# Optimization experiments

Hardware: AMD Instinct MI355X
Metric: run time of the kernel (lower is better)

## Reference

```python
import jax, jax.numpy as jnp
import numpy as np

NUM_CLASSES = 100
CLUSTERS_PER_CLASS = 64
LATENT_DIM = 128
BATCH = 32768


def setup_inputs() -> dict:
    key = jax.random.key(0)
    kx, kc, kl = jax.random.split(key, 3)
    x = jax.random.normal(kx, (BATCH, LATENT_DIM), dtype=jnp.float32)
    # nn.Parameter(torch.randn(C, Kc, D) * 0.1)
    centers = jax.random.normal(kc, (NUM_CLASSES, CLUSTERS_PER_CLASS, LATENT_DIM), dtype=jnp.float32) * 0.1
    labels = jax.random.randint(kl, (BATCH,), 0, NUM_CLASSES, dtype=jnp.int64)
    return {"x": x, "centers": centers, "labels": labels}


def reference(x, centers, labels):
    # [C, Kc, D] -> [K, D]
    all_centers = centers.reshape(-1, LATENT_DIM).astype(x.dtype)
    x2 = jnp.sum(x * x, axis=-1, keepdims=True)            # [B,1]
    c2 = jnp.sum(all_centers * all_centers, axis=-1)       # [K]
    sq = x2 + c2[None, :] - 2.0 * jnp.einsum('bd,kd->bk', x, all_centers)
    distances = jnp.sqrt(jnp.maximum(sq, 0.0))             # [B,K]
    closest_indices = jnp.argmin(distances, axis=1)        # [B]
    class_predictions = closest_indices // CLUSTERS_PER_CLASS
    cluster_assignments = closest_indices % CLUSTERS_PER_CLASS
    quantized_hard = all_centers[closest_indices]          # [B,D]
    min_distances = jnp.take_along_axis(distances, closest_indices[:, None], axis=1)[:, 0]
    # straight-through estimator (training path in the torch module)
    quantized = x + jax.lax.stop_gradient(quantized_hard - x)
    return quantized, cluster_assignments, min_distances, class_predictions
```

## Files before the change

### kernel.cpp

```cpp
#include <hip/hip_runtime.h>
#include <math.h>

#define BATCH  32768
#define D      128
#define K      6400
#define KC     64
#define ROWS_PER_BLOCK 128
#define CHUNK_C 128
#define NCHUNKS 50

typedef _Float16 half8 __attribute__((ext_vector_type(8)));
typedef float    floatx4 __attribute__((ext_vector_type(4)));

typedef __attribute__((address_space(3))) unsigned       lds_uint;
typedef __attribute__((address_space(1))) const unsigned glb_uint;

__device__ __forceinline__ void async_lds16(const void* g, void* l) {
    __builtin_amdgcn_global_load_lds((glb_uint*)g, (lds_uint*)l, 16, 0, 0);
}

__global__ __launch_bounds__(256) void pack_kernel(const float* __restrict__ centers,
                                                   _Float16* __restrict__ wh,
                                                   float* __restrict__ c2n) {
    int tid = blockIdx.x * 256 + threadIdx.x;
    int ch = tid >> 11;
    int u  = (tid >> 7) & 15;
    int cw = tid & 127;
    int center = ch * CHUNK_C + cw;
    const float* src = centers + (size_t)center * D + u * 8;
    float4 a = *(const float4*)src;
    float4 b = *(const float4*)(src + 4);
    float f[8] = {a.x, a.y, a.z, a.w, b.x, b.y, b.z, b.w};
    half8 h;
#pragma unroll
    for (int j = 0; j < 8; ++j) h[j] = (_Float16)f[j];
    *(half8*)(wh + (size_t)tid * 8) = h;

    if (blockIdx.x < K / KC) {
        int c_local = threadIdx.x >> 2, part = threadIdx.x & 3;
        int c = blockIdx.x * 64 + c_local;
        const float4* p = (const float4*)(centers + (size_t)c * D + part * 32);
        float s = 0.f;
#pragma unroll
        for (int i = 0; i < 8; ++i) {
            float4 v = p[i];
            s = fmaf(v.x, v.x, s); s = fmaf(v.y, v.y, s);
            s = fmaf(v.z, v.z, s); s = fmaf(v.w, v.w, s);
        }
        s += __shfl_xor(s, 1, 64);
        s += __shfl_xor(s, 2, 64);
        if (part == 0) c2n[c] = -0.5f * s;
    }
}

__global__ __launch_bounds__(1024, 4) void dist_kernel(
    const float* __restrict__ x, const float* __restrict__ centers,
    const _Float16* __restrict__ wh, const float* __restrict__ c2n,
    float* __restrict__ out) {
    __shared__ char lds[65536];

    const int t    = threadIdx.x;
    const int w    = t >> 6;
    const int L    = t & 63;
    const int quad = L >> 4;
    const int n16  = L & 15;
    const int cq   = w & 3;
    const int rq   = w >> 2;
    const int gr0  = blockIdx.x * ROWS_PER_BLOCK;

    half8 Ah[2][4];
#pragma unroll
    for (int rt = 0; rt < 2; ++rt) {
        int r = gr0 + rq * 32 + rt * 16 + n16;
        const float* xr = x + (size_t)r * D + quad * 8;
#pragma unroll
        for (int ks = 0; ks < 4; ++ks) {
            float4 a = *(const float4*)(xr + ks * 32);
            float4 b = *(const float4*)(xr + ks * 32 + 4);
            float f[8] = {a.x, a.y, a.z, a.w, b.x, b.y, b.z, b.w};
            half8 h;
#pragma unroll
            for (int j = 0; j < 8; ++j) h[j] = (_Float16)f[j];
            Ah[rt][ks] = h;
        }
    }

    float b1[8], b2[8];
#pragma unroll
    for (int k = 0; k < 8; ++k) { b1[k] = -1e30f; b2[k] = -1e30f; }

    const char* gh = (const char*)wh;

#pragma unroll
    for (int i = 0; i < 2; ++i) {
        int seg = w * 2 + i;
        async_lds16(gh + seg * 1024 + L * 16, lds + seg * 1024);
    }

    float c2vA[2], c2vB[2];
#pragma unroll
    for (int ct = 0; ct < 2; ++ct) c2vA[ct] = c2n[cq * 32 + ct * 16 + n16];
    __syncthreads();

    for (int ci = 0; ci < NCHUNKS; ++ci) {
        const char* cur = lds + (ci & 1) * 32768;
        if (ci + 1 < NCHUNKS) {
            const char* gn = gh + (size_t)(ci + 1) * 32768;
            char* nxt = lds + ((ci + 1) & 1) * 32768;
#pragma unroll
            for (int i = 0; i < 2; ++i) {
                int seg = w * 2 + i;
                async_lds16(gn + seg * 1024 + L * 16, nxt + seg * 1024);
            }
            const int kb1 = (ci + 1) * CHUNK_C + cq * 32;
#pragma unroll
            for (int ct = 0; ct < 2; ++ct) c2vB[ct] = c2n[kb1 + ct * 16 + n16];
        }

        floatx4 acc[2][2];
#pragma unroll
        for (int rt = 0; rt < 2; ++rt)
#pragma unroll
            for (int ct = 0; ct < 2; ++ct)
                acc[rt][ct] = (floatx4){c2vA[ct], c2vA[ct], c2vA[ct], c2vA[ct]};

        __builtin_amdgcn_s_setprio(1);
#pragma unroll
        for (int ks = 0; ks < 4; ++ks) {
            const half8* pb = (const half8*)cur + (ks * 4 + quad) * 128 + cq * 32 + n16;
#pragma unroll
            for (int ct = 0; ct < 2; ++ct) {
                half8 Bf = pb[ct * 16];
                acc[0][ct] = __builtin_amdgcn_mfma_f32_16x16x32_f16(Ah[0][ks], Bf, acc[0][ct], 0, 0, 0);
                acc[1][ct] = __builtin_amdgcn_mfma_f32_16x16x32_f16(Ah[1][ks], Bf, acc[1][ct], 0, 0, 0);
            }
        }
        __builtin_amdgcn_s_setprio(0);

        const unsigned pk0 = (unsigned)(2 * ci);
        const unsigned pk1 = (unsigned)(2 * ci + 1);
#pragma unroll
        for (int rt = 0; rt < 2; ++rt)
#pragma unroll
            for (int reg = 0; reg < 4; ++reg) {
                int k = rt * 4 + reg;
                float v0 = __uint_as_float((__float_as_uint(acc[rt][0][reg]) & ~127u) | pk0);
                float v1 = __uint_as_float((__float_as_uint(acc[rt][1][reg]) & ~127u) | pk1);
                float v  = fmaxf(v0, v1);
                b2[k] = __builtin_amdgcn_fmed3f(b1[k], b2[k], v);
                b1[k] = fmaxf(b1[k], v);
            }

#pragma unroll
        for (int ct = 0; ct < 2; ++ct) c2vA[ct] = c2vB[ct];

        __syncthreads();
    }

    int* candL = (int*)lds;

#pragma unroll
    for (int k = 0; k < 8; ++k) {
        unsigned u1 = __float_as_uint(b1[k]), u2 = __float_as_uint(b2[k]);
        int e1 = (int)(u1 & 127u), e2 = (int)(u2 & 127u);
        int p1 = (e1 >> 1) * 128 + cq * 32 + (e1 & 1) * 16 + n16;
        int p2 = (e2 >> 1) * 128 + cq * 32 + (e2 & 1) * 16 + n16;
        float v1 = b1[k], v2 = b2[k];
#pragma unroll
        for (int m = 1; m < 16; m <<= 1) {
            float o1 = __shfl_xor(v1, m, 64), o2 = __shfl_xor(v2, m, 64);
            int   q1 = __shfl_xor(p1, m, 64), q2 = __shfl_xor(p2, m, 64);
            bool firstMine = (v1 > o1) || (v1 == o1 && p1 < q1);
            float nv1 = firstMine ? v1 : o1;  int np1 = firstMine ? p1 : q1;
            float cb  = firstMine ? o1 : v1;  int cpi = firstMine ? q1 : p1;
            float ob  = firstMine ? v2 : o2;  int obi = firstMine ? p2 : q2;
            bool secOwn = (ob > cb) || (ob == cb && obi < cpi);
            v1 = nv1; p1 = np1;
            v2 = secOwn ? ob : cb;  p2 = secOwn ? obi : cpi;
        }
        if (n16 == 0) {
            int rloc = rq * 32 + (k >> 2) * 16 + quad * 4 + (k & 3);
            candL[rloc * 8 + cq * 2 + 0] = p1;
            candL[rloc * 8 + cq * 2 + 1] = p2;
        }
    }
    __syncthreads();

    {
        int r = t >> 3, p = t & 7;
        int row = gr0 + r;
        int ix = candL[r * 8 + p];
        const float4* xr4 = (const float4*)(x + (size_t)row * D);
        const float4* c4  = (const float4*)(centers + (size_t)ix * D);
        float dot = 0.f, x2s = 0.f, c2 = 0.f;
#pragma unroll
        for (int d4 = 0; d4 < 32; ++d4) {
            float4 xv = xr4[d4], cv = c4[d4];
            dot = fmaf(xv.x, cv.x, dot); dot = fmaf(xv.y, cv.y, dot);
            dot = fmaf(xv.z, cv.z, dot); dot = fmaf(xv.w, cv.w, dot);
            x2s = fmaf(xv.x, xv.x, x2s); x2s = fmaf(xv.y, xv.y, x2s);
            x2s = fmaf(xv.z, xv.z, x2s); x2s = fmaf(xv.w, xv.w, x2s);
            c2  = fmaf(cv.x, cv.x, c2);  c2  = fmaf(cv.y, cv.y, c2);
            c2  = fmaf(cv.z, cv.z, c2);  c2  = fmaf(cv.w, cv.w, c2);
        }
        float sq = x2s + c2 - 2.f * dot;
#pragma unroll
        for (int m = 1; m < 8; m <<= 1) {
            float osq = __shfl_xor(sq, m, 64);
            int   oix = __shfl_xor(ix, m, 64);
            if (osq < sq || (osq == sq && oix < ix)) { sq = osq; ix = oix; }
        }

        float* out_clu = out + (size_t)BATCH * D;
        float* out_md  = out_clu + BATCH;
        float* out_cls = out_md + BATCH;
        if (p == 0) {
            out_md[row]  = sqrtf(fmaxf(sq, 0.f));
            out_clu[row] = (float)(ix & (KC - 1));
            out_cls[row] = (float)(ix >> 6);
        }

        const float4* cv4 = (const float4*)(centers + (size_t)ix * D) + p * 4;
        const float4* xv4 = (const float4*)(x + (size_t)row * D) + p * 4;
        float4* o4 = (float4*)(out + (size_t)row * D) + p * 4;
#pragma unroll
        for (int i = 0; i < 4; ++i) {
            float4 cv = cv4[i], xv = xv4[i];
            float4 o;
            o.x = xv.x + (cv.x - xv.x);
            o.y = xv.y + (cv.y - xv.y);
            o.z = xv.z + (cv.z - xv.z);
            o.w = xv.w + (cv.w - xv.w);
            o4[i] = o;
        }
    }
}

extern "C" void kernel_launch(void* const* d_in, const int* in_sizes, int n_in,
                              void* d_out, int out_size, void* d_ws, size_t ws_size,
                              hipStream_t stream) {
    const float* x       = (const float*)d_in[0];
    const float* centers = (const float*)d_in[1];
    float* out = (float*)d_out;

    _Float16* wh  = (_Float16*)d_ws;
    float*    c2n = (float*)(wh + (size_t)K * D);

    pack_kernel<<<(K * 16) / 256, 256, 0, stream>>>(centers, wh, c2n);
    dist_kernel<<<BATCH / ROWS_PER_BLOCK, 1024, 0, stream>>>(x, centers, wh, c2n, out);
}
```

Measured before the change: 173.1 us.

## Remap waves to 8 column groups by 1 row group with 4 row tiles each

Changes the per-wave tile from 2 row tiles by 2 column tiles to 4 row tiles by 1 column tile. Each wave now covers 64 rows and 16 centers per chunk, so every B fragment read from LDS feeds four MFMAs instead of two, and the A fragments are held in more registers. The chunk index packed into the low mantissa bits no longer needs a column-tile bit. The candidate list grows to 16 per row, and each exact-refinement thread now scores two candidates. Risks are higher register pressure from 16 A fragments and 16-entry top-2 arrays under the 1024-thread launch bound, plus roughly twice the refinement gathers.

```diff
diff --git a/kernel.cpp b/kernel.cpp
--- a/kernel.cpp
+++ b/kernel.cpp
@@ -64,14 +64,15 @@
     const int L    = t & 63;
     const int quad = L >> 4;
     const int n16  = L & 15;
-    const int cq   = w & 3;
-    const int rq   = w >> 2;
+    const int cq   = w & 7;
+    const int rq   = w >> 3;
     const int gr0  = blockIdx.x * ROWS_PER_BLOCK;
-
-    half8 Ah[2][4];
-#pragma unroll
-    for (int rt = 0; rt < 2; ++rt) {
-        int r = gr0 + rq * 32 + rt * 16 + n16;
+    const int laneC = cq * 16 + n16;
+
+    half8 Ah[4][4];
+#pragma unroll
+    for (int rt = 0; rt < 4; ++rt) {
+        int r = gr0 + rq * 64 + rt * 16 + n16;
         const float* xr = x + (size_t)r * D + quad * 8;
 #pragma unroll
         for (int ks = 0; ks < 4; ++ks) {
@@ -85,9 +86,9 @@
         }
     }
 
-    float b1[8], b2[8];
-#pragma unroll
-    for (int k = 0; k < 8; ++k) { b1[k] = -1e30f; b2[k] = -1e30f; }
+    float b1[16], b2[16];
+#pragma unroll
+    for (int k = 0; k < 16; ++k) { b1[k] = -1e30f; b2[k] = -1e30f; }
 
     const char* gh = (const char*)wh;
 
@@ -97,9 +98,7 @@
         async_lds16(gh + seg * 1024 + L * 16, lds + seg * 1024);
     }
 
-    float c2vA[2], c2vB[2];
-#pragma unroll
-    for (int ct = 0; ct < 2; ++ct) c2vA[ct] = c2n[cq * 32 + ct * 16 + n16];
+    float c2vA = c2n[laneC], c2vB;
     __syncthreads();
 
     for (int ci = 0; ci < NCHUNKS; ++ci) {
@@ -112,47 +111,38 @@
                 int seg = w * 2 + i;
                 async_lds16(gn + seg * 1024 + L * 16, nxt + seg * 1024);
             }
-            const int kb1 = (ci + 1) * CHUNK_C + cq * 32;
-#pragma unroll
-            for (int ct = 0; ct < 2; ++ct) c2vB[ct] = c2n[kb1 + ct * 16 + n16];
-        }
-
-        floatx4 acc[2][2];
-#pragma unroll
-        for (int rt = 0; rt < 2; ++rt)
-#pragma unroll
-            for (int ct = 0; ct < 2; ++ct)
-                acc[rt][ct] = (floatx4){c2vA[ct], c2vA[ct], c2vA[ct], c2vA[ct]};
+            c2vB = c2n[(ci + 1) * CHUNK_C + laneC];
+        }
+
+        floatx4 acc[4];
+#pragma unroll
+        for (int rt = 0; rt < 4; ++rt)
+            acc[rt] = (floatx4){c2vA, c2vA, c2vA, c2vA};
 
         __builtin_amdgcn_s_setprio(1);
 #pragma unroll
         for (int ks = 0; ks < 4; ++ks) {
-            const half8* pb = (const half8*)cur + (ks * 4 + quad) * 128 + cq * 32 + n16;
-#pragma unroll
-            for (int ct = 0; ct < 2; ++ct) {
-                half8 Bf = pb[ct * 16];
-                acc[0][ct] = __builtin_amdgcn_mfma_f32_16x16x32_f16(Ah[0][ks], Bf, acc[0][ct], 0, 0, 0);
-                acc[1][ct] = __builtin_amdgcn_mfma_f32_16x16x32_f16(Ah[1][ks], Bf, acc[1][ct], 0, 0, 0);
-            }
+            const half8* pb = (const half8*)cur + (ks * 4 + quad) * 128 + laneC;
+            half8 Bf = pb[0];
+            acc[0] = __builtin_amdgcn_mfma_f32_16x16x32_f16(Ah[0][ks], Bf, acc[0], 0, 0, 0);
+            acc[1] = __builtin_amdgcn_mfma_f32_16x16x32_f16(Ah[1][ks], Bf, acc[1], 0, 0, 0);
+            acc[2] = __builtin_amdgcn_mfma_f32_16x16x32_f16(Ah[2][ks], Bf, acc[2], 0, 0, 0);
+            acc[3] = __builtin_amdgcn_mfma_f32_16x16x32_f16(Ah[3][ks], Bf, acc[3], 0, 0, 0);
         }
         __builtin_amdgcn_s_setprio(0);
 
-        const unsigned pk0 = (unsigned)(2 * ci);
-        const unsigned pk1 = (unsigned)(2 * ci + 1);
-#pragma unroll
-        for (int rt = 0; rt < 2; ++rt)
+        const unsigned pk = (unsigned)ci;
+#pragma unroll
+        for (int rt = 0; rt < 4; ++rt)
 #pragma unroll
             for (int reg = 0; reg < 4; ++reg) {
                 int k = rt * 4 + reg;
-                float v0 = __uint_as_float((__float_as_uint(acc[rt][0][reg]) & ~127u) | pk0);
-                float v1 = __uint_as_float((__float_as_uint(acc[rt][1][reg]) & ~127u) | pk1);
-                float v  = fmaxf(v0, v1);
+                float v = __uint_as_float((__float_as_uint(acc[rt][reg]) & ~127u) | pk);
                 b2[k] = __builtin_amdgcn_fmed3f(b1[k], b2[k], v);
                 b1[k] = fmaxf(b1[k], v);
             }
 
-#pragma unroll
-        for (int ct = 0; ct < 2; ++ct) c2vA[ct] = c2vB[ct];
+        c2vA = c2vB;
 
         __syncthreads();
     }
@@ -160,11 +150,11 @@
     int* candL = (int*)lds;
 
 #pragma unroll
-    for (int k = 0; k < 8; ++k) {
+    for (int k = 0; k < 16; ++k) {
         unsigned u1 = __float_as_uint(b1[k]), u2 = __float_as_uint(b2[k]);
         int e1 = (int)(u1 & 127u), e2 = (int)(u2 & 127u);
-        int p1 = (e1 >> 1) * 128 + cq * 32 + (e1 & 1) * 16 + n16;
-        int p2 = (e2 >> 1) * 128 + cq * 32 + (e2 & 1) * 16 + n16;
+        int p1 = e1 * CHUNK_C + laneC;
+        int p2 = e2 * CHUNK_C + laneC;
         float v1 = b1[k], v2 = b2[k];
 #pragma unroll
         for (int m = 1; m < 16; m <<= 1) {
@@ -179,9 +169,9 @@
             v2 = secOwn ? ob : cb;  p2 = secOwn ? obi : cpi;
         }
         if (n16 == 0) {
-            int rloc = rq * 32 + (k >> 2) * 16 + quad * 4 + (k & 3);
-            candL[rloc * 8 + cq * 2 + 0] = p1;
-            candL[rloc * 8 + cq * 2 + 1] = p2;
+            int rloc = rq * 64 + (k >> 2) * 16 + quad * 4 + (k & 3);
+            candL[rloc * 16 + cq * 2 + 0] = p1;
+            candL[rloc * 16 + cq * 2 + 1] = p2;
         }
     }
     __syncthreads();
@@ -189,21 +179,31 @@
     {
         int r = t >> 3, p = t & 7;
         int row = gr0 + r;
-        int ix = candL[r * 8 + p];
+        int ixa = candL[r * 16 + p * 2 + 0];
+        int ixb = candL[r * 16 + p * 2 + 1];
         const float4* xr4 = (const float4*)(x + (size_t)row * D);
-        const float4* c4  = (const float4*)(centers + (size_t)ix * D);
-        float dot = 0.f, x2s = 0.f, c2 = 0.f;
+        const float4* ca4 = (const float4*)(centers + (size_t)ixa * D);
+        const float4* cb4 = (const float4*)(centers + (size_t)ixb * D);
+        float dota = 0.f, dotb = 0.f, x2s = 0.f, c2a = 0.f, c2b = 0.f;
 #pragma unroll
         for (int d4 = 0; d4 < 32; ++d4) {
-            float4 xv = xr4[d4], cv = c4[d4];
-            dot = fmaf(xv.x, cv.x, dot); dot = fmaf(xv.y, cv.y, dot);
-            dot = fmaf(xv.z, cv.z, dot); dot = fmaf(xv.w, cv.w, dot);
+            float4 xv = xr4[d4], av = ca4[d4], bv = cb4[d4];
+            dota = fmaf(xv.x, av.x, dota); dota = fmaf(xv.y, av.y, dota);
+            dota = fmaf(xv.z, av.z, dota); dota = fmaf(xv.w, av.w, dota);
+            dotb = fmaf(xv.x, bv.x, dotb); dotb = fmaf(xv.y, bv.y, dotb);
+            dotb = fmaf(xv.z, bv.z, dotb); dotb = fmaf(xv.w, bv.w, dotb);
             x2s = fmaf(xv.x, xv.x, x2s); x2s = fmaf(xv.y, xv.y, x2s);
             x2s = fmaf(xv.z, xv.z, x2s); x2s = fmaf(xv.w, xv.w, x2s);
-            c2  = fmaf(cv.x, cv.x, c2);  c2  = fmaf(cv.y, cv.y, c2);
-            c2  = fmaf(cv.z, cv.z, c2);  c2  = fmaf(cv.w, cv.w, c2);
-        }
-        float sq = x2s + c2 - 2.f * dot;
+            c2a = fmaf(av.x, av.x, c2a); c2a = fmaf(av.y, av.y, c2a);
+            c2a = fmaf(av.z, av.z, c2a); c2a = fmaf(av.w, av.w, c2a);
+            c2b = fmaf(bv.x, bv.x, c2b); c2b = fmaf(bv.y, bv.y, c2b);
+            c2b = fmaf(bv.z, bv.z, c2b); c2b = fmaf(bv.w, bv.w, c2b);
+        }
+        float sqa = x2s + c2a - 2.f * dota;
+        float sqb = x2s + c2b - 2.f * dotb;
+        bool aw = (sqa < sqb) || (sqa == sqb && ixa < ixb);
+        float sq = aw ? sqa : sqb;
+        int   ix = aw ? ixa : ixb;
 #pragma unroll
         for (int m = 1; m < 8; m <<= 1) {
             float osq = __shfl_xor(sq, m, 64);
```

After: 265.9 us. 53.6% more time.

## Switch distance GEMM from 16x16x32 to 32x32x16 MFMA tiles

Applied to the files above, without the earlier changes.

Each wave now computes its 32x32 tile with eight 32x32x16 f16 MFMAs instead of sixteen 16x16x32 MFMAs, which changes the A/B fragment layout, the LDS read pattern, and the per-lane top-2 tracking (16 accumulator registers per lane, chunk index packed in the low mantissa bits). Each B fragment is read once per k-step instead of being shared across two row tiles, and fewer MFMA issues are needed. In exchange the final top-2 reduction takes an extra shuffle stage (over 32 lanes), and the top-2 state doubles to 16 values per lane, which raises register pressure at 1024 threads per block.

```diff
diff --git a/kernel.cpp b/kernel.cpp
--- a/kernel.cpp
+++ b/kernel.cpp
@@ -10,7 +10,7 @@
 #define NCHUNKS 50
 
 typedef _Float16 half8 __attribute__((ext_vector_type(8)));
-typedef float    floatx4 __attribute__((ext_vector_type(4)));
+typedef float    floatx16 __attribute__((ext_vector_type(16)));
 
 typedef __attribute__((address_space(3))) unsigned       lds_uint;
 typedef __attribute__((address_space(1))) const unsigned glb_uint;
@@ -24,10 +24,10 @@
                                                    float* __restrict__ c2n) {
     int tid = blockIdx.x * 256 + threadIdx.x;
     int ch = tid >> 11;
-    int u  = (tid >> 7) & 15;
+    int kb = (tid >> 7) & 15;
     int cw = tid & 127;
     int center = ch * CHUNK_C + cw;
-    const float* src = centers + (size_t)center * D + u * 8;
+    const float* src = centers + (size_t)center * D + kb * 8;
     float4 a = *(const float4*)src;
     float4 b = *(const float4*)(src + 4);
     float f[8] = {a.x, a.y, a.z, a.w, b.x, b.y, b.z, b.w};
@@ -59,35 +59,35 @@
     float* __restrict__ out) {
     __shared__ char lds[65536];
 
-    const int t    = threadIdx.x;
-    const int w    = t >> 6;
-    const int L    = t & 63;
-    const int quad = L >> 4;
-    const int n16  = L & 15;
-    const int cq   = w & 3;
-    const int rq   = w >> 2;
-    const int gr0  = blockIdx.x * ROWS_PER_BLOCK;
-
-    half8 Ah[2][4];
-#pragma unroll
-    for (int rt = 0; rt < 2; ++rt) {
-        int r = gr0 + rq * 32 + rt * 16 + n16;
-        const float* xr = x + (size_t)r * D + quad * 8;
-#pragma unroll
-        for (int ks = 0; ks < 4; ++ks) {
-            float4 a = *(const float4*)(xr + ks * 32);
-            float4 b = *(const float4*)(xr + ks * 32 + 4);
+    const int t   = threadIdx.x;
+    const int w   = t >> 6;
+    const int L   = t & 63;
+    const int col = L & 31;
+    const int hi  = L >> 5;
+    const int cq  = w & 3;
+    const int rq  = w >> 2;
+    const int gr0 = blockIdx.x * ROWS_PER_BLOCK;
+    const int laneC = cq * 32 + col;
+
+    half8 Ah[8];
+    {
+        int r = gr0 + rq * 32 + col;
+        const float* xr = x + (size_t)r * D + hi * 8;
+#pragma unroll
+        for (int ks = 0; ks < 8; ++ks) {
+            float4 a = *(const float4*)(xr + ks * 16);
+            float4 b = *(const float4*)(xr + ks * 16 + 4);
             float f[8] = {a.x, a.y, a.z, a.w, b.x, b.y, b.z, b.w};
             half8 h;
 #pragma unroll
             for (int j = 0; j < 8; ++j) h[j] = (_Float16)f[j];
-            Ah[rt][ks] = h;
-        }
-    }
-
-    float b1[8], b2[8];
-#pragma unroll
-    for (int k = 0; k < 8; ++k) { b1[k] = -1e30f; b2[k] = -1e30f; }
+            Ah[ks] = h;
+        }
+    }
+
+    float b1[16], b2[16];
+#pragma unroll
+    for (int k = 0; k < 16; ++k) { b1[k] = -1e30f; b2[k] = -1e30f; }
 
     const char* gh = (const char*)wh;
 
@@ -97,9 +97,7 @@
         async_lds16(gh + seg * 1024 + L * 16, lds + seg * 1024);
     }
 
-    float c2vA[2], c2vB[2];
-#pragma unroll
-    for (int ct = 0; ct < 2; ++ct) c2vA[ct] = c2n[cq * 32 + ct * 16 + n16];
+    float c2vA = c2n[laneC], c2vB;
     __syncthreads();
 
     for (int ci = 0; ci < NCHUNKS; ++ci) {
@@ -112,47 +110,30 @@
                 int seg = w * 2 + i;
                 async_lds16(gn + seg * 1024 + L * 16, nxt + seg * 1024);
             }
-            const int kb1 = (ci + 1) * CHUNK_C + cq * 32;
-#pragma unroll
-            for (int ct = 0; ct < 2; ++ct) c2vB[ct] = c2n[kb1 + ct * 16 + n16];
-        }
-
-        floatx4 acc[2][2];
-#pragma unroll
-        for (int rt = 0; rt < 2; ++rt)
-#pragma unroll
-            for (int ct = 0; ct < 2; ++ct)
-                acc[rt][ct] = (floatx4){c2vA[ct], c2vA[ct], c2vA[ct], c2vA[ct]};
+            c2vB = c2n[(ci + 1) * CHUNK_C + laneC];
+        }
+
+        floatx16 acc;
+#pragma unroll
+        for (int r = 0; r < 16; ++r) acc[r] = c2vA;
 
         __builtin_amdgcn_s_setprio(1);
 #pragma unroll
-        for (int ks = 0; ks < 4; ++ks) {
-            const half8* pb = (const half8*)cur + (ks * 4 + quad) * 128 + cq * 32 + n16;
-#pragma unroll
-            for (int ct = 0; ct < 2; ++ct) {
-                half8 Bf = pb[ct * 16];
-                acc[0][ct] = __builtin_amdgcn_mfma_f32_16x16x32_f16(Ah[0][ks], Bf, acc[0][ct], 0, 0, 0);
-                acc[1][ct] = __builtin_amdgcn_mfma_f32_16x16x32_f16(Ah[1][ks], Bf, acc[1][ct], 0, 0, 0);
-            }
+        for (int ks = 0; ks < 8; ++ks) {
+            half8 Bf = *(const half8*)(cur + (((2 * ks + hi) << 7) + laneC) * 16);
+            acc = __builtin_amdgcn_mfma_f32_32x32x16_f16(Ah[ks], Bf, acc, 0, 0, 0);
         }
         __builtin_amdgcn_s_setprio(0);
 
-        const unsigned pk0 = (unsigned)(2 * ci);
-        const unsigned pk1 = (unsigned)(2 * ci + 1);
-#pragma unroll
-        for (int rt = 0; rt < 2; ++rt)
-#pragma unroll
-            for (int reg = 0; reg < 4; ++reg) {
-                int k = rt * 4 + reg;
-                float v0 = __uint_as_float((__float_as_uint(acc[rt][0][reg]) & ~127u) | pk0);
-                float v1 = __uint_as_float((__float_as_uint(acc[rt][1][reg]) & ~127u) | pk1);
-                float v  = fmaxf(v0, v1);
-                b2[k] = __builtin_amdgcn_fmed3f(b1[k], b2[k], v);
-                b1[k] = fmaxf(b1[k], v);
-            }
-
-#pragma unroll
-        for (int ct = 0; ct < 2; ++ct) c2vA[ct] = c2vB[ct];
+        const unsigned pk = (unsigned)ci;
+#pragma unroll
+        for (int reg = 0; reg < 16; ++reg) {
+            float v = __uint_as_float((__float_as_uint(acc[reg]) & ~127u) | pk);
+            b2[reg] = __builtin_amdgcn_fmed3f(b1[reg], b2[reg], v);
+            b1[reg] = fmaxf(b1[reg], v);
+        }
+
+        c2vA = c2vB;
 
         __syncthreads();
     }
@@ -160,14 +141,14 @@
     int* candL = (int*)lds;
 
 #pragma unroll
-    for (int k = 0; k < 8; ++k) {
-        unsigned u1 = __float_as_uint(b1[k]), u2 = __float_as_uint(b2[k]);
+    for (int reg = 0; reg < 16; ++reg) {
+        unsigned u1 = __float_as_uint(b1[reg]), u2 = __float_as_uint(b2[reg]);
         int e1 = (int)(u1 & 127u), e2 = (int)(u2 & 127u);
-        int p1 = (e1 >> 1) * 128 + cq * 32 + (e1 & 1) * 16 + n16;
-        int p2 = (e2 >> 1) * 128 + cq * 32 + (e2 & 1) * 16 + n16;
-        float v1 = b1[k], v2 = b2[k];
-#pragma unroll
-        for (int m = 1; m < 16; m <<= 1) {
+        int p1 = e1 * CHUNK_C + laneC;
+        int p2 = e2 * CHUNK_C + laneC;
+        float v1 = b1[reg], v2 = b2[reg];
+#pragma unroll
+        for (int m = 1; m < 32; m <<= 1) {
             float o1 = __shfl_xor(v1, m, 64), o2 = __shfl_xor(v2, m, 64);
             int   q1 = __shfl_xor(p1, m, 64), q2 = __shfl_xor(p2, m, 64);
             bool firstMine = (v1 > o1) || (v1 == o1 && p1 < q1);
@@ -178,8 +159,8 @@
             v1 = nv1; p1 = np1;
             v2 = secOwn ? ob : cb;  p2 = secOwn ? obi : cpi;
         }
-        if (n16 == 0) {
-            int rloc = rq * 32 + (k >> 2) * 16 + quad * 4 + (k & 3);
+        if (col == 0) {
+            int rloc = rq * 32 + (reg & 3) + 8 * (reg >> 2) + 4 * hi;
             candL[rloc * 8 + cq * 2 + 0] = p1;
             candL[rloc * 8 + cq * 2 + 1] = p2;
         }
```

Measured after the change: 200.2 us. +15.7%, slower.
